# Kernel optimization log

Hardware: AMD Instinct MI355X
Metric: run time of the kernel (lower is better)

Reference implementation:

```python
import jax, jax.numpy as jnp
import numpy as np

DIM = 1024
B, L = 4, 4096


def setup_inputs() -> dict:
    key = jax.random.key(0)
    ks = jax.random.split(key, 6)
    s = 1.0 / np.sqrt(DIM)
    x = jax.random.normal(ks[0], (B, L, DIM), dtype=jnp.float32)
    Wk = jax.random.uniform(ks[1], (DIM, DIM), jnp.float32, -s, s)
    bk = jax.random.uniform(ks[2], (DIM,), jnp.float32, -s, s)
    Wv = jax.random.uniform(ks[3], (DIM, DIM), jnp.float32, -s, s)
    bv = jax.random.uniform(ks[4], (DIM,), jnp.float32, -s, s)
    ln_g = jnp.ones((DIM,), jnp.float32)
    ln_b = jnp.zeros((DIM,), jnp.float32)
    Wo = jax.random.uniform(ks[5], (DIM, DIM), jnp.float32, -s, s)
    bo = jnp.zeros((DIM,), jnp.float32)
    return {"x": x, "Wk": Wk, "bk": bk, "Wv": Wv, "bv": bv,
            "ln_g": ln_g, "ln_b": ln_b, "Wo": Wo, "bo": bo}


def reference(x, Wk, bk, Wv, bv, ln_g, ln_b, Wo, bo):
    B_, L_, D = x.shape
    # key/value projections (torch Linear: x @ W.T + b)
    keys = x @ Wk.T + bk
    keys = keys / jnp.maximum(jnp.linalg.norm(keys, axis=-1, keepdims=True), 1e-12)
    values = x @ Wv.T + bv
    # circular convolution via FFT: bind keys with values
    Kf = jnp.fft.rfft(keys, axis=-1)
    Vf = jnp.fft.rfft(values, axis=-1)
    bound = jnp.fft.irfft(Kf * Vf, n=D, axis=-1)
    # cumulative holographic memory over sequence
    memory = jnp.cumsum(bound, axis=1)
    # circular correlation (unbind): conj of key spectrum
    Mf = jnp.fft.rfft(memory, axis=-1)
    retrieved = jnp.fft.irfft(Mf * jnp.conj(Kf), n=D, axis=-1)
    # position-dependent normalization: sqrt(1..L)
    norm = jnp.sqrt(jnp.arange(1, L_ + 1, dtype=x.dtype)).reshape(1, L_, 1)
    r = retrieved / norm
    # LayerNorm (eps=1e-5) + output Linear
    mu = jnp.mean(r, axis=-1, keepdims=True)
    var = jnp.var(r, axis=-1, keepdims=True)
    r_ln = (r - mu) * jax.lax.rsqrt(var + 1e-5) * ln_g + ln_b
    return x + (r_ln @ Wo.T + bo)
```

## Files before the change

### kernel.cpp

```cpp
#include <hip/hip_runtime.h>
#include <math.h>

#define B_SZ 4
#define L_SZ 4096
#define D_SZ 1024
#define M_SZ (B_SZ * L_SZ)
#define NBINS 513
#define CCH   (2 * NBINS)
#define TCH 32
#define TLEN (L_SZ / TCH)

typedef short bf16x8 __attribute__((ext_vector_type(8)));
typedef float f32x4  __attribute__((ext_vector_type(4)));
typedef unsigned short us8 __attribute__((ext_vector_type(8)));

#define AS1 __attribute__((address_space(1)))
#define AS3 __attribute__((address_space(3)))

__device__ inline unsigned short f2bf(float f) {
    unsigned int u = __float_as_uint(f);
    u += 0x7fffu + ((u >> 16) & 1u);
    return (unsigned short)(u >> 16);
}

__global__ __launch_bounds__(256) void cast_f32_bf16(
        const float* __restrict__ in, unsigned short* __restrict__ out, int n8) {
    int i = blockIdx.x * 256 + threadIdx.x;
    if (i >= n8) return;
    const float4* p = (const float4*)in + 2 * (size_t)i;
    float4 a = p[0], b = p[1];
    us8 o;
    o[0] = f2bf(a.x); o[1] = f2bf(a.y); o[2] = f2bf(a.z); o[3] = f2bf(a.w);
    o[4] = f2bf(b.x); o[5] = f2bf(b.y); o[6] = f2bf(b.z); o[7] = f2bf(b.w);
    *(us8*)(out + (size_t)i * 8) = o;
}

__global__ __launch_bounds__(256) void cast_w3(
        const float* __restrict__ Wk, const float* __restrict__ Wv,
        const float* __restrict__ Wo,
        unsigned short* __restrict__ WB, unsigned short* __restrict__ Wob, int n8) {
    int i = blockIdx.x * 256 + threadIdx.x;
    if (i >= n8) return;
    const int which = blockIdx.y;
    const float* src = (which == 0) ? Wk : (which == 1) ? Wv : Wo;
    unsigned short* dst = (which == 0) ? WB : (which == 1) ? (WB + D_SZ * D_SZ) : Wob;
    const float4* p = (const float4*)src + 2 * (size_t)i;
    float4 a = p[0], b = p[1];
    us8 o;
    o[0] = f2bf(a.x); o[1] = f2bf(a.y); o[2] = f2bf(a.z); o[3] = f2bf(a.w);
    o[4] = f2bf(b.x); o[5] = f2bf(b.y); o[6] = f2bf(b.z); o[7] = f2bf(b.w);
    *(us8*)(dst + (size_t)i * 8) = o;
}

template<int CNT>
__global__ __launch_bounds__(512, 4) void gemm_mfma(
        const unsigned short* __restrict__ A, const unsigned short* __restrict__ W,
        const float* __restrict__ bias0, const float* __restrict__ bias1,
        const float* __restrict__ resid,
        float* __restrict__ C0, float* __restrict__ C1, int M, int K) {
    __shared__ unsigned short Abuf[3][256 * 32];
    __shared__ unsigned short Bbuf[3][128 * 32];
    const int id   = blockIdx.x;
    const int bx   = (id >> 3) % CNT;
    const int by   = (id & 7) + 8 * (id / (8 * CNT));
    const int tid  = threadIdx.x;
    const int lane = tid & 63;
    const int wid  = tid >> 6;
    const int wr   = wid >> 2;
    const int wc   = wid & 3;
    const int bm   = by * 256;
    const int bn   = bx * 128;

    const int sl = tid >> 3;
    const int sq = (tid & 7) ^ (sl & 7);
    const int srow = 2 * sl + (sq >> 2);
    const int skof = (sq & 3) * 8;
    const unsigned short* Abase = A + (size_t)(bm + srow) * K + skof;
    const unsigned short* Wbase = W + (size_t)(bn + srow) * K + skof;
    const int dstoff = tid * 16;

    auto stage3 = [&](int slot, int kk) {
        __builtin_amdgcn_global_load_lds((const AS1 unsigned int*)(Abase + kk),
            (AS3 unsigned int*)((char*)&Abuf[slot][0] + dstoff), 16, 0, 0);
        __builtin_amdgcn_global_load_lds((const AS1 unsigned int*)(Abase + (size_t)128 * K + kk),
            (AS3 unsigned int*)((char*)&Abuf[slot][128 * 32] + dstoff), 16, 0, 0);
        __builtin_amdgcn_global_load_lds((const AS1 unsigned int*)(Wbase + kk),
            (AS3 unsigned int*)((char*)&Bbuf[slot][0] + dstoff), 16, 0, 0);
    };

    const int fr = lane & 15;
    const int kq = lane >> 4;
    const int rslot = (((((fr & 1) << 2) + kq) ^ ((fr >> 1) & 7)) << 4);
    const int aoff0 = wr * 8192 + (fr >> 1) * 128 + rslot;
    const int boff0 = wc * 2048 + (fr >> 1) * 128 + rslot;

    f32x4 acc[8][2] = {};

    const int nt = K >> 5;
    stage3(0, 0);
    stage3(1, 32);
    asm volatile("s_waitcnt vmcnt(3)" ::: "memory");
    __builtin_amdgcn_s_barrier();
    asm volatile("" ::: "memory");

    int slot = 0, slot2 = 2;
    for (int cur = 0; cur < nt; ++cur) {
        bf16x8 a[8], b[2];
        const char* Ab = (const char*)&Abuf[slot][0];
        const char* Bb = (const char*)&Bbuf[slot][0];
        #pragma unroll
        for (int nf = 0; nf < 2; nf++)
            b[nf] = *(const bf16x8*)(Bb + boff0 + nf * 1024);
        #pragma unroll
        for (int mf = 0; mf < 8; mf++)
            a[mf] = *(const bf16x8*)(Ab + aoff0 + mf * 1024);
        if (cur + 2 < nt) stage3(slot2, (cur + 2) << 5);
        __builtin_amdgcn_s_setprio(1);
        #pragma unroll
        for (int mf = 0; mf < 8; mf++)
            #pragma unroll
            for (int nf = 0; nf < 2; nf++)
                acc[mf][nf] = __builtin_amdgcn_mfma_f32_16x16x32_bf16(
                                  a[mf], b[nf], acc[mf][nf], 0, 0, 0);
        __builtin_amdgcn_s_setprio(0);
        if (cur + 2 < nt) { asm volatile("s_waitcnt vmcnt(3)" ::: "memory"); }
        else              { asm volatile("s_waitcnt vmcnt(0)" ::: "memory"); }
        __builtin_amdgcn_s_barrier();
        asm volatile("" ::: "memory");
        slot  = (slot  == 2) ? 0 : slot  + 1;
        slot2 = (slot2 == 2) ? 0 : slot2 + 1;
    }

    const int col0 = lane & 15;
    const int quad = lane >> 4;
    #pragma unroll
    for (int nf = 0; nf < 2; nf++) {
        const int ng = bn + wc * 32 + nf * 16 + col0;
        const int half = ng >> 10;
        const int n = ng & 1023;
        float* __restrict__ Cp = half ? C1 : C0;
        const float bv = half ? bias1[n] : bias0[n];
        #pragma unroll
        for (int mf = 0; mf < 8; mf++) {
            #pragma unroll
            for (int r = 0; r < 4; r++) {
                const int m = bm + wr * 128 + mf * 16 + quad * 4 + r;
                float v = acc[mf][nf][r] + bv;
                size_t off = (size_t)m * 1024 + n;
                if (resid) v += resid[off];
                Cp[off] = v;
            }
        }
    }
}

#define SWZ(a) ((a) ^ (((a) >> 4) & 15))

struct cplx { float r, i; };
__device__ inline cplx cmul(cplx a, cplx b) {
    return {a.r * b.r - a.i * b.i, a.r * b.i + a.i * b.r};
}

__device__ inline void r4bfly(cplx v[4], float s) {
    cplx t0 {v[0].r + v[2].r, v[0].i + v[2].i};
    cplx t1 {v[0].r - v[2].r, v[0].i - v[2].i};
    cplx t2 {v[1].r + v[3].r, v[1].i + v[3].i};
    cplx t3 {v[1].r - v[3].r, v[1].i - v[3].i};
    cplx j3 {-s * t3.i, s * t3.r};
    v[0] = {t0.r + t2.r, t0.i + t2.i};
    v[2] = {t0.r - t2.r, t0.i - t2.i};
    v[1] = {t1.r + j3.r, t1.i + j3.i};
    v[3] = {t1.r - j3.r, t1.i - j3.i};
}

template<int SIGN>
__device__ inline void fft1024_r(float2* bA, float2* bB, cplx v[4], int tid) {
    const float s = (float)SIGN;
    r4bfly(v, s);
    {
        const int base = tid << 2;
        #pragma unroll
        for (int e = 0; e < 4; e++)
            bA[SWZ(base + e)] = make_float2(v[e].r, v[e].i);
    }
    __syncthreads();
    float2* cur = bA;
    float2* nxt = bB;
    #pragma unroll
    for (int q = 1; q <= 3; q++) {
        const int Ls = 1 << (2 * q);
        #pragma unroll
        for (int k = 0; k < 4; k++) {
            float2 t = cur[SWZ(tid + (k << 8))];
            v[k] = {t.x, t.y};
        }
        const int d = tid & (Ls - 1);
        const float ang = s * 1.57079632679489662f * (float)d / (float)Ls;
        float sn, cs; __sincosf(ang, &sn, &cs);
        cplx w1 {cs, sn};
        cplx w2 = cmul(w1, w1);
        cplx w3 = cmul(w2, w1);
        v[1] = cmul(v[1], w1);
        v[2] = cmul(v[2], w2);
        v[3] = cmul(v[3], w3);
        r4bfly(v, s);
        const int base = ((tid >> (2 * q)) << (2 * q + 2)) + d;
        #pragma unroll
        for (int e = 0; e < 4; e++)
            nxt[SWZ(base + (e << (2 * q)))] = make_float2(v[e].r, v[e].i);
        float2* tmp = cur; cur = nxt; nxt = tmp;
        __syncthreads();
    }
    #pragma unroll
    for (int k = 0; k < 4; k++) {
        float2 t = cur[SWZ(tid + (k << 8))];
        v[k] = {t.x, t.y};
    }
    {
        const float ang = s * 1.57079632679489662f * (float)tid / 256.0f;
        float sn, cs; __sincosf(ang, &sn, &cs);
        cplx w1 {cs, sn};
        cplx w2 = cmul(w1, w1);
        cplx w3 = cmul(w2, w1);
        v[1] = cmul(v[1], w1);
        v[2] = cmul(v[2], w2);
        v[3] = cmul(v[3], w3);
        r4bfly(v, s);
    }
}

__global__ __launch_bounds__(256) void bind_fft_kernel(
        float* __restrict__ KIO, const float* __restrict__ V,
        float* __restrict__ P) {
    __shared__ float2 bA[1024], bB[1024];
    __shared__ float red[256];
    const int token = blockIdx.x;
    const int tid = threadIdx.x;

    float* krow = KIO + (size_t)token * D_SZ;
    const float* vrow = V + (size_t)token * D_SZ;
    float kv[4], vv[4];
    float ss = 0.0f;
    #pragma unroll
    for (int k = 0; k < 4; k++) {
        kv[k] = krow[tid + (k << 8)];
        vv[k] = vrow[tid + (k << 8)];
        ss += kv[k] * kv[k];
    }
    red[tid] = ss;
    __syncthreads();
    for (int sft = 128; sft > 0; sft >>= 1) {
        if (tid < sft) red[tid] += red[tid + sft];
        __syncthreads();
    }
    const float scale = 1.0f / fmaxf(sqrtf(red[0]), 1e-12f);

    cplx z[4];
    #pragma unroll
    for (int k = 0; k < 4; k++) z[k] = {kv[k] * scale, vv[k]};

    __syncthreads();
    fft1024_r<-1>(bA, bB, z, tid);

    #pragma unroll
    for (int e = 0; e < 4; e++)
        bA[SWZ(tid + (e << 8))] = make_float2(z[e].r, z[e].i);
    __syncthreads();

    float2* Po = (float2*)(P + (size_t)token * CCH);
    for (int bin = tid; bin < NBINS; bin += 256) {
        float2 Zb = bA[SWZ(bin)];
        float2 Zm = bA[SWZ((1024 - bin) & 1023)];
        float ar = 0.5f * (Zb.x + Zm.x);
        float ai = 0.5f * (Zb.y - Zm.y);
        float br = 0.5f * (Zb.y + Zm.y);
        float bi = 0.5f * (Zm.x - Zb.x);
        Po[bin] = make_float2(ar * br - ai * bi, ar * bi + ai * br);
        if (bin == 0)        krow[0] = ar;
        else if (bin == 512) krow[1] = ar;
        else { krow[2 * bin] = ar; krow[2 * bin + 1] = ai; }
    }
}

__global__ __launch_bounds__(256) void cumsum_local(
        float* __restrict__ S, float* __restrict__ totals) {
    const int c = blockIdx.x * 256 + threadIdx.x;
    if (c >= CCH) return;
    const int chunk = blockIdx.y;
    const int b = blockIdx.z;
    size_t p = ((size_t)b * L_SZ + (size_t)chunk * TLEN) * CCH + c;
    float acc = 0.0f;
    #pragma unroll 4
    for (int t = 0; t < TLEN; t++) {
        acc += S[p];
        S[p] = acc;
        p += CCH;
    }
    totals[((size_t)b * TCH + chunk) * CCH + c] = acc;
}

__global__ __launch_bounds__(256) void scan_totals(float* __restrict__ totals) {
    const int c = blockIdx.x * 256 + threadIdx.x;
    if (c >= CCH) return;
    const int b = blockIdx.y;
    float acc = 0.0f;
    for (int ch = 0; ch < TCH; ch++) {
        size_t idx = ((size_t)b * TCH + ch) * CCH + c;
        float v = totals[idx];
        totals[idx] = acc;
        acc += v;
    }
}

__global__ __launch_bounds__(256) void unbind_ln_kernel(
        const float* __restrict__ P, const float* __restrict__ totals,
        const float* __restrict__ KF,
        const float* __restrict__ ln_g, const float* __restrict__ ln_b,
        unsigned short* __restrict__ RLNb) {
    __shared__ float2 bA[1024], bB[1024];
    __shared__ float red1[256], red2[256];
    const int token = blockIdx.x;
    const int tid = threadIdx.x;
    const int b = token >> 12;
    const int t = token & (L_SZ - 1);
    const int chunk = t >> 7;

    const float* kfrow   = KF + (size_t)token * D_SZ;
    const float2* Srow   = (const float2*)(P + (size_t)token * CCH);
    const float2* offrow = (const float2*)(totals + ((size_t)b * TCH + chunk) * CCH);
    #pragma unroll
    for (int e = 0; e < 3; e++) {
        const int bin = tid + (e << 8);
        if (bin < NBINS) {
            float kr, ki;
            if (bin == 0)        { kr = kfrow[0]; ki = 0.0f; }
            else if (bin == 512) { kr = kfrow[1]; ki = 0.0f; }
            else { float2 kf2 = *(const float2*)(kfrow + 2 * bin); kr = kf2.x; ki = kf2.y; }
            float2 s2 = Srow[bin];
            float2 o2 = offrow[bin];
            float sr = s2.x + o2.x, si = s2.y + o2.y;
            bA[SWZ(bin)] = make_float2(sr * kr + si * ki, si * kr - sr * ki);
        }
    }
    __syncthreads();
    for (int n = 513 + tid; n < 1024; n += 256) {
        float2 c = bA[SWZ(1024 - n)];
        bA[SWZ(n)] = make_float2(c.x, -c.y);
    }
    __syncthreads();

    cplx rz[4];
    #pragma unroll
    for (int k = 0; k < 4; k++) {
        float2 c = bA[SWZ(tid + (k << 8))];
        rz[k] = {c.x, c.y};
    }
    __syncthreads();
    fft1024_r<1>(bA, bB, rz, tid);

    const float posscale = (1.0f / 1024.0f) * rsqrtf((float)(t + 1));
    float rv[4];
    float sum = 0.0f, sumsq = 0.0f;
    #pragma unroll
    for (int e = 0; e < 4; e++) {
        float v = rz[e].r * posscale;
        rv[e] = v;
        sum += v;
        sumsq += v * v;
    }
    red1[tid] = sum; red2[tid] = sumsq;
    __syncthreads();
    for (int sft = 128; sft > 0; sft >>= 1) {
        if (tid < sft) { red1[tid] += red1[tid + sft]; red2[tid] += red2[tid + sft]; }
        __syncthreads();
    }
    const float mu = red1[0] * (1.0f / 1024.0f);
    const float var = red2[0] * (1.0f / 1024.0f) - mu * mu;
    const float rstd = rsqrtf(var + 1e-5f);

    unsigned short* outp = RLNb + (size_t)token * D_SZ;
    #pragma unroll
    for (int e = 0; e < 4; e++) {
        const int d = tid + (e << 8);
        outp[d] = f2bf((rv[e] - mu) * rstd * ln_g[d] + ln_b[d]);
    }
}

extern "C" void kernel_launch(void* const* d_in, const int* in_sizes, int n_in,
                              void* d_out, int out_size, void* d_ws, size_t ws_size,
                              hipStream_t stream) {
    (void)in_sizes; (void)n_in; (void)out_size; (void)ws_size;
    const float* x    = (const float*)d_in[0];
    const float* Wk   = (const float*)d_in[1];
    const float* bk   = (const float*)d_in[2];
    const float* Wv   = (const float*)d_in[3];
    const float* bv   = (const float*)d_in[4];
    const float* ln_g = (const float*)d_in[5];
    const float* ln_b = (const float*)d_in[6];
    const float* Wo   = (const float*)d_in[7];
    const float* bo   = (const float*)d_in[8];
    float* out = (float*)d_out;

    char* w = (char*)d_ws;
    float* Kraw   = (float*)w;  w += (size_t)M_SZ * D_SZ * 4;
    float* V      = (float*)w;  w += (size_t)M_SZ * D_SZ * 4;
    float* P      = (float*)w;  w += (size_t)M_SZ * CCH * 4;
    float* totals = (float*)w;  w += (size_t)B_SZ * TCH * CCH * 4;
    unsigned short* xb  = (unsigned short*)w;  w += (size_t)M_SZ * D_SZ * 2;
    unsigned short* WB  = (unsigned short*)w;  w += (size_t)2 * D_SZ * D_SZ * 2;
    unsigned short* Wob = (unsigned short*)w;  w += (size_t)D_SZ * D_SZ * 2;
    unsigned short* RLNb = (unsigned short*)V;

    const int n8x = M_SZ * D_SZ / 8;
    const int n8w = D_SZ * D_SZ / 8;
    cast_f32_bf16<<<n8x / 256, 256, 0, stream>>>(x, xb, n8x);
    dim3 wgrid(n8w / 256, 3);
    cast_w3<<<wgrid, 256, 0, stream>>>(Wk, Wv, Wo, WB, Wob, n8w);

    gemm_mfma<16><<<(M_SZ / 256) * 16, 512, 0, stream>>>(
        xb, WB, bk, bv, nullptr, Kraw, V, M_SZ, D_SZ);

    bind_fft_kernel<<<M_SZ, 256, 0, stream>>>(Kraw, V, P);

    dim3 cgrid((CCH + 255) / 256, TCH, B_SZ);
    cumsum_local<<<cgrid, 256, 0, stream>>>(P, totals);
    dim3 sgrid((CCH + 255) / 256, B_SZ);
    scan_totals<<<sgrid, 256, 0, stream>>>(totals);

    unbind_ln_kernel<<<M_SZ, 256, 0, stream>>>(P, totals, Kraw, ln_g, ln_b, RLNb);

    gemm_mfma<8><<<(M_SZ / 256) * 8, 512, 0, stream>>>(
        RLNb, Wob, bo, bo, x, out, out, M_SZ, D_SZ);
}
```

Baseline: 426.9 us.

## Fuse local cumsum into bind FFT and pack two tokens per inverse FFT

The bind kernel now processes 16 consecutive tokens per block. It accumulates the per-bin running sum in registers and writes prefix sums directly, which removes the separate cumsum pass that read and rewrote the spectrum buffer. The chunk-offset scan becomes two-level (16-token chunks, then groups of 16). The unbind kernel packs two real inverse FFTs into one complex FFT, and reductions use wavefront shuffles instead of shared-memory trees. In exchange there are fewer blocks in the bind kernel, the per-token loop is serial, and the totals arrays are larger.

```diff
diff --git a/kernel.cpp b/kernel.cpp
--- a/kernel.cpp
+++ b/kernel.cpp
@@ -7,8 +7,9 @@
 #define M_SZ (B_SZ * L_SZ)
 #define NBINS 513
 #define CCH   (2 * NBINS)
-#define TCH 32
-#define TLEN (L_SZ / TCH)
+#define TLEN 16
+#define NCH  (L_SZ / TLEN)
+#define NG   16
 
 typedef short bf16x8 __attribute__((ext_vector_type(8)));
 typedef float f32x4  __attribute__((ext_vector_type(4)));
@@ -229,160 +230,218 @@
     }
 }
 
-__global__ __launch_bounds__(256) void bind_fft_kernel(
+__global__ __launch_bounds__(256) void bind_cum_kernel(
         float* __restrict__ KIO, const float* __restrict__ V,
-        float* __restrict__ P) {
+        float* __restrict__ P, float* __restrict__ totals) {
     __shared__ float2 bA[1024], bB[1024];
-    __shared__ float red[256];
-    const int token = blockIdx.x;
+    __shared__ float red[4];
+    const int blk = blockIdx.x;
     const int tid = threadIdx.x;
-
-    float* krow = KIO + (size_t)token * D_SZ;
-    const float* vrow = V + (size_t)token * D_SZ;
-    float kv[4], vv[4];
-    float ss = 0.0f;
-    #pragma unroll
-    for (int k = 0; k < 4; k++) {
-        kv[k] = krow[tid + (k << 8)];
-        vv[k] = vrow[tid + (k << 8)];
-        ss += kv[k] * kv[k];
-    }
-    red[tid] = ss;
-    __syncthreads();
-    for (int sft = 128; sft > 0; sft >>= 1) {
-        if (tid < sft) red[tid] += red[tid + sft];
+    const int wv  = tid >> 6;
+    const int ln  = tid & 63;
+    const size_t tok0 = (size_t)blk * TLEN;
+
+    float r0r = 0.f, r0i = 0.f, r1r = 0.f, r1i = 0.f, r2r = 0.f, r2i = 0.f;
+
+    float kvC[4], vvC[4];
+    {
+        const float* krow = KIO + tok0 * D_SZ;
+        const float* vrow = V   + tok0 * D_SZ;
+        #pragma unroll
+        for (int k = 0; k < 4; k++) {
+            kvC[k] = krow[tid + (k << 8)];
+            vvC[k] = vrow[tid + (k << 8)];
+        }
+    }
+
+    for (int tk = 0; tk < TLEN; ++tk) {
+        const size_t token = tok0 + tk;
+        float* krow = KIO + token * D_SZ;
+
+        float ss = 0.f;
+        #pragma unroll
+        for (int k = 0; k < 4; k++) ss += kvC[k] * kvC[k];
+        #pragma unroll
+        for (int m = 1; m < 64; m <<= 1) ss += __shfl_xor(ss, m, 64);
+        if (ln == 0) red[wv] = ss;
         __syncthreads();
-    }
-    const float scale = 1.0f / fmaxf(sqrtf(red[0]), 1e-12f);
-
-    cplx z[4];
-    #pragma unroll
-    for (int k = 0; k < 4; k++) z[k] = {kv[k] * scale, vv[k]};
-
-    __syncthreads();
-    fft1024_r<-1>(bA, bB, z, tid);
-
-    #pragma unroll
-    for (int e = 0; e < 4; e++)
-        bA[SWZ(tid + (e << 8))] = make_float2(z[e].r, z[e].i);
-    __syncthreads();
-
-    float2* Po = (float2*)(P + (size_t)token * CCH);
-    for (int bin = tid; bin < NBINS; bin += 256) {
-        float2 Zb = bA[SWZ(bin)];
-        float2 Zm = bA[SWZ((1024 - bin) & 1023)];
-        float ar = 0.5f * (Zb.x + Zm.x);
-        float ai = 0.5f * (Zb.y - Zm.y);
-        float br = 0.5f * (Zb.y + Zm.y);
-        float bi = 0.5f * (Zm.x - Zb.x);
-        Po[bin] = make_float2(ar * br - ai * bi, ar * bi + ai * br);
-        if (bin == 0)        krow[0] = ar;
-        else if (bin == 512) krow[1] = ar;
-        else { krow[2 * bin] = ar; krow[2 * bin + 1] = ai; }
-    }
-}
-
-__global__ __launch_bounds__(256) void cumsum_local(
-        float* __restrict__ S, float* __restrict__ totals) {
+        const float scale = 1.0f /
+            fmaxf(sqrtf(red[0] + red[1] + red[2] + red[3]), 1e-12f);
+
+        cplx z[4];
+        #pragma unroll
+        for (int k = 0; k < 4; k++) z[k] = {kvC[k] * scale, vvC[k]};
+
+        if (tk + 1 < TLEN) {
+            const float* krowN = KIO + (token + 1) * D_SZ;
+            const float* vrowN = V   + (token + 1) * D_SZ;
+            #pragma unroll
+            for (int k = 0; k < 4; k++) {
+                kvC[k] = krowN[tid + (k << 8)];
+                vvC[k] = vrowN[tid + (k << 8)];
+            }
+        }
+
+        fft1024_r<-1>(bA, bB, z, tid);
+
+        #pragma unroll
+        for (int e = 0; e < 4; e++)
+            bA[SWZ(tid + (e << 8))] = make_float2(z[e].r, z[e].i);
+        __syncthreads();
+
+        float2* Po = (float2*)(P + token * CCH);
+        auto procbin = [&](int bin, float& rr, float& ri) {
+            float2 Zb = bA[SWZ(bin)];
+            float2 Zm = bA[SWZ((1024 - bin) & 1023)];
+            float ar = 0.5f * (Zb.x + Zm.x);
+            float ai = 0.5f * (Zb.y - Zm.y);
+            float br = 0.5f * (Zb.y + Zm.y);
+            float bi = 0.5f * (Zm.x - Zb.x);
+            rr += ar * br - ai * bi;
+            ri += ar * bi + ai * br;
+            Po[bin] = make_float2(rr, ri);
+            if (bin == 0)        krow[0] = ar;
+            else if (bin == 512) krow[1] = ar;
+            else { krow[2 * bin] = ar; krow[2 * bin + 1] = ai; }
+        };
+        procbin(tid,       r0r, r0i);
+        procbin(tid + 256, r1r, r1i);
+        if (tid == 0) procbin(512, r2r, r2i);
+    }
+
+    float* trow = totals + (size_t)blk * CCH;
+    trow[2 * tid]             = r0r;  trow[2 * tid + 1]         = r0i;
+    trow[2 * (tid + 256)]     = r1r;  trow[2 * (tid + 256) + 1] = r1i;
+    if (tid == 0) { trow[1024] = r2r; trow[1025] = r2i; }
+}
+
+__global__ __launch_bounds__(256) void scan_s1(
+        float* __restrict__ totals, float* __restrict__ gt) {
     const int c = blockIdx.x * 256 + threadIdx.x;
     if (c >= CCH) return;
-    const int chunk = blockIdx.y;
+    const int g = blockIdx.y;
     const int b = blockIdx.z;
-    size_t p = ((size_t)b * L_SZ + (size_t)chunk * TLEN) * CCH + c;
-    float acc = 0.0f;
-    #pragma unroll 4
-    for (int t = 0; t < TLEN; t++) {
-        acc += S[p];
-        S[p] = acc;
-        p += CCH;
-    }
-    totals[((size_t)b * TCH + chunk) * CCH + c] = acc;
-}
-
-__global__ __launch_bounds__(256) void scan_totals(float* __restrict__ totals) {
+    float run = 0.f;
+    #pragma unroll
+    for (int i = 0; i < 16; i++) {
+        size_t idx = ((size_t)(b * NCH + g * 16 + i)) * CCH + c;
+        float v = totals[idx];
+        totals[idx] = run;
+        run += v;
+    }
+    gt[((size_t)(b * NG + g)) * CCH + c] = run;
+}
+
+__global__ __launch_bounds__(256) void scan_s2(float* __restrict__ gt) {
     const int c = blockIdx.x * 256 + threadIdx.x;
     if (c >= CCH) return;
     const int b = blockIdx.y;
-    float acc = 0.0f;
-    for (int ch = 0; ch < TCH; ch++) {
-        size_t idx = ((size_t)b * TCH + ch) * CCH + c;
-        float v = totals[idx];
-        totals[idx] = acc;
-        acc += v;
-    }
-}
-
-__global__ __launch_bounds__(256) void unbind_ln_kernel(
+    float run = 0.f;
+    #pragma unroll
+    for (int g = 0; g < NG; g++) {
+        size_t idx = ((size_t)(b * NG + g)) * CCH + c;
+        float v = gt[idx];
+        gt[idx] = run;
+        run += v;
+    }
+}
+
+__global__ __launch_bounds__(256) void unbind2_ln_kernel(
         const float* __restrict__ P, const float* __restrict__ totals,
-        const float* __restrict__ KF,
+        const float* __restrict__ gt, const float* __restrict__ KF,
         const float* __restrict__ ln_g, const float* __restrict__ ln_b,
         unsigned short* __restrict__ RLNb) {
     __shared__ float2 bA[1024], bB[1024];
-    __shared__ float red1[256], red2[256];
-    const int token = blockIdx.x;
-    const int tid = threadIdx.x;
-    const int b = token >> 12;
-    const int t = token & (L_SZ - 1);
-    const int chunk = t >> 7;
-
-    const float* kfrow   = KF + (size_t)token * D_SZ;
-    const float2* Srow   = (const float2*)(P + (size_t)token * CCH);
-    const float2* offrow = (const float2*)(totals + ((size_t)b * TCH + chunk) * CCH);
-    #pragma unroll
-    for (int e = 0; e < 3; e++) {
-        const int bin = tid + (e << 8);
-        if (bin < NBINS) {
-            float kr, ki;
-            if (bin == 0)        { kr = kfrow[0]; ki = 0.0f; }
-            else if (bin == 512) { kr = kfrow[1]; ki = 0.0f; }
-            else { float2 kf2 = *(const float2*)(kfrow + 2 * bin); kr = kf2.x; ki = kf2.y; }
-            float2 s2 = Srow[bin];
-            float2 o2 = offrow[bin];
-            float sr = s2.x + o2.x, si = s2.y + o2.y;
-            bA[SWZ(bin)] = make_float2(sr * kr + si * ki, si * kr - sr * ki);
-        }
-    }
+    __shared__ float red[16];
+    const int pair = blockIdx.x;
+    const int tid  = threadIdx.x;
+    const int wv   = tid >> 6;
+    const int ln   = tid & 63;
+    const size_t ta = (size_t)pair * 2, tb = ta + 1;
+    const int bidx = (int)(ta >> 12);
+    const int t_a  = (int)(ta & (L_SZ - 1));
+    const int chunk = t_a >> 4;
+
+    const float2* Sa2  = (const float2*)(P + ta * CCH);
+    const float2* Sb2  = (const float2*)(P + tb * CCH);
+    const float*  Ka   = KF + ta * D_SZ;
+    const float*  Kb   = KF + tb * D_SZ;
+    const float2* off2 = (const float2*)(totals + (size_t)(bidx * NCH + chunk) * CCH);
+    const float2* gof2 = (const float2*)(gt + (size_t)(bidx * NG + (chunk >> 4)) * CCH);
+
+    auto zc = [&](int bin, const float2* S2, const float* kf, float2 og) {
+        float kr, ki;
+        if (bin == 0)        { kr = kf[0]; ki = 0.f; }
+        else if (bin == 512) { kr = kf[1]; ki = 0.f; }
+        else { float2 k2 = *(const float2*)(kf + 2 * bin); kr = k2.x; ki = k2.y; }
+        float2 s2 = S2[bin];
+        float sr = s2.x + og.x, si = s2.y + og.y;
+        return make_float2(sr * kr + si * ki, si * kr - sr * ki);
+    };
+    auto fill = [&](int bin) {
+        float2 o = off2[bin], g = gof2[bin];
+        float2 og = make_float2(o.x + g.x, o.y + g.y);
+        float2 Za = zc(bin, Sa2, Ka, og);
+        float2 Zb = zc(bin, Sb2, Kb, og);
+        bA[SWZ(bin)] = make_float2(Za.x - Zb.y, Za.y + Zb.x);
+        if (bin != 0 && bin != 512)
+            bA[SWZ(1024 - bin)] = make_float2(Za.x + Zb.y, Zb.x - Za.y);
+    };
+    fill(tid);
+    fill(tid + 256);
+    if (tid == 0) fill(512);
     __syncthreads();
-    for (int n = 513 + tid; n < 1024; n += 256) {
-        float2 c = bA[SWZ(1024 - n)];
-        bA[SWZ(n)] = make_float2(c.x, -c.y);
-    }
-    __syncthreads();
-
-    cplx rz[4];
+
+    cplx z[4];
     #pragma unroll
     for (int k = 0; k < 4; k++) {
         float2 c = bA[SWZ(tid + (k << 8))];
-        rz[k] = {c.x, c.y};
+        z[k] = {c.x, c.y};
     }
     __syncthreads();
-    fft1024_r<1>(bA, bB, rz, tid);
-
-    const float posscale = (1.0f / 1024.0f) * rsqrtf((float)(t + 1));
-    float rv[4];
-    float sum = 0.0f, sumsq = 0.0f;
+    fft1024_r<1>(bA, bB, z, tid);
+
+    const float sa = (1.0f / 1024.0f) * rsqrtf((float)(t_a + 1));
+    const float sb = (1.0f / 1024.0f) * rsqrtf((float)(t_a + 2));
+    float ra[4], rb[4];
+    float s1a = 0.f, s2a = 0.f, s1b = 0.f, s2b = 0.f;
     #pragma unroll
     for (int e = 0; e < 4; e++) {
-        float v = rz[e].r * posscale;
-        rv[e] = v;
-        sum += v;
-        sumsq += v * v;
-    }
-    red1[tid] = sum; red2[tid] = sumsq;
+        ra[e] = z[e].r * sa;
+        rb[e] = z[e].i * sb;
+        s1a += ra[e]; s2a += ra[e] * ra[e];
+        s1b += rb[e]; s2b += rb[e] * rb[e];
+    }
+    #pragma unroll
+    for (int m = 1; m < 64; m <<= 1) {
+        s1a += __shfl_xor(s1a, m, 64);
+        s2a += __shfl_xor(s2a, m, 64);
+        s1b += __shfl_xor(s1b, m, 64);
+        s2b += __shfl_xor(s2b, m, 64);
+    }
+    if (ln == 0) {
+        red[wv] = s1a; red[4 + wv] = s2a; red[8 + wv] = s1b; red[12 + wv] = s2b;
+    }
     __syncthreads();
-    for (int sft = 128; sft > 0; sft >>= 1) {
-        if (tid < sft) { red1[tid] += red1[tid + sft]; red2[tid] += red2[tid + sft]; }
-        __syncthreads();
-    }
-    const float mu = red1[0] * (1.0f / 1024.0f);
-    const float var = red2[0] * (1.0f / 1024.0f) - mu * mu;
-    const float rstd = rsqrtf(var + 1e-5f);
-
-    unsigned short* outp = RLNb + (size_t)token * D_SZ;
+    const float S1a = red[0] + red[1] + red[2] + red[3];
+    const float S2a = red[4] + red[5] + red[6] + red[7];
+    const float S1b = red[8] + red[9] + red[10] + red[11];
+    const float S2b = red[12] + red[13] + red[14] + red[15];
+    const float mua = S1a * (1.0f / 1024.0f);
+    const float vara = S2a * (1.0f / 1024.0f) - mua * mua;
+    const float rsa = rsqrtf(vara + 1e-5f);
+    const float mub = S1b * (1.0f / 1024.0f);
+    const float varb = S2b * (1.0f / 1024.0f) - mub * mub;
+    const float rsb = rsqrtf(varb + 1e-5f);
+
+    unsigned short* outA = RLNb + ta * D_SZ;
+    unsigned short* outB = RLNb + tb * D_SZ;
     #pragma unroll
     for (int e = 0; e < 4; e++) {
         const int d = tid + (e << 8);
-        outp[d] = f2bf((rv[e] - mu) * rstd * ln_g[d] + ln_b[d]);
+        const float g = ln_g[d], be = ln_b[d];
+        outA[d] = f2bf((ra[e] - mua) * rsa * g + be);
+        outB[d] = f2bf((rb[e] - mub) * rsb * g + be);
     }
 }
 
@@ -405,7 +464,8 @@
     float* Kraw   = (float*)w;  w += (size_t)M_SZ * D_SZ * 4;
     float* V      = (float*)w;  w += (size_t)M_SZ * D_SZ * 4;
     float* P      = (float*)w;  w += (size_t)M_SZ * CCH * 4;
-    float* totals = (float*)w;  w += (size_t)B_SZ * TCH * CCH * 4;
+    float* totals = (float*)w;  w += (size_t)B_SZ * NCH * CCH * 4;
+    float* gt     = (float*)w;  w += (size_t)B_SZ * NG * CCH * 4;
     unsigned short* xb  = (unsigned short*)w;  w += (size_t)M_SZ * D_SZ * 2;
     unsigned short* WB  = (unsigned short*)w;  w += (size_t)2 * D_SZ * D_SZ * 2;
     unsigned short* Wob = (unsigned short*)w;  w += (size_t)D_SZ * D_SZ * 2;
@@ -420,14 +480,15 @@
     gemm_mfma<16><<<(M_SZ / 256) * 16, 512, 0, stream>>>(
         xb, WB, bk, bv, nullptr, Kraw, V, M_SZ, D_SZ);
 
-    bind_fft_kernel<<<M_SZ, 256, 0, stream>>>(Kraw, V, P);
-
-    dim3 cgrid((CCH + 255) / 256, TCH, B_SZ);
-    cumsum_local<<<cgrid, 256, 0, stream>>>(P, totals);
-    dim3 sgrid((CCH + 255) / 256, B_SZ);
-    scan_totals<<<sgrid, 256, 0, stream>>>(totals);
-
-    unbind_ln_kernel<<<M_SZ, 256, 0, stream>>>(P, totals, Kraw, ln_g, ln_b, RLNb);
+    bind_cum_kernel<<<M_SZ / TLEN, 256, 0, stream>>>(Kraw, V, P, totals);
+
+    dim3 g1((CCH + 255) / 256, NG, B_SZ);
+    scan_s1<<<g1, 256, 0, stream>>>(totals, gt);
+    dim3 g2((CCH + 255) / 256, B_SZ);
+    scan_s2<<<g2, 256, 0, stream>>>(gt);
+
+    unbind2_ln_kernel<<<M_SZ / 2, 256, 0, stream>>>(
+        P, totals, gt, Kraw, ln_g, ln_b, RLNb);
 
     gemm_mfma<8><<<(M_SZ / 256) * 8, 512, 0, stream>>>(
         RLNb, Wob, bo, bo, x, out, out, M_SZ, D_SZ);
```

After: 417.4 us. 1.02x faster.
